# Performance work log

Hardware: AMD Instinct MI355X
Metric: run time of the kernel (lower is better)

Reference implementation:

```python
import jax, jax.numpy as jnp
import numpy as np

N = 100000
E = 1600000
IN_DIM = 128
OUT_DIM = 128
EDGE_DIM = 4
LN_EPS = 1e-5


def setup_inputs() -> dict:
    key = jax.random.key(0)
    ks = jax.random.split(key, 12)
    s_in = 1.0 / np.sqrt(IN_DIM)
    s_ed = 1.0 / np.sqrt(EDGE_DIM)
    s_out = 1.0 / np.sqrt(OUT_DIM)
    s_cat = 1.0 / np.sqrt(IN_DIM + OUT_DIM)
    return {
        "x": jax.random.normal(ks[0], (N, IN_DIM), jnp.float32),
        "edge_index": jax.random.randint(ks[1], (2, E), 0, N, jnp.int32),
        "edge_attr": jax.random.normal(ks[2], (E, EDGE_DIM), jnp.float32),
        # agg_mlp: Linear(in_dim, out_dim)
        "agg_W": jax.random.uniform(ks[3], (IN_DIM, OUT_DIM), jnp.float32, -s_in, s_in),
        "agg_b": jnp.zeros((OUT_DIM,), jnp.float32),
        # edge_mlp: Linear(edge_dim, out_dim) -> SiLU -> Linear(out_dim, 1) -> Sigmoid
        "edge_W1": jax.random.uniform(ks[4], (EDGE_DIM, OUT_DIM), jnp.float32, -s_ed, s_ed),
        "edge_b1": jnp.zeros((OUT_DIM,), jnp.float32),
        "edge_W2": jax.random.uniform(ks[5], (OUT_DIM, 1), jnp.float32, -s_out, s_out),
        "edge_b2": jnp.zeros((1,), jnp.float32),
        # update_mlp: Linear(in+out, out) -> SiLU -> Linear(out, out)
        "upd_W1": jax.random.uniform(ks[6], (IN_DIM + OUT_DIM, OUT_DIM), jnp.float32, -s_cat, s_cat),
        "upd_b1": jnp.zeros((OUT_DIM,), jnp.float32),
        "upd_W2": jax.random.uniform(ks[7], (OUT_DIM, OUT_DIM), jnp.float32, -s_out, s_out),
        "upd_b2": jnp.zeros((OUT_DIM,), jnp.float32),
        # LayerNorm(out_dim)
        "ln_g": jnp.ones((OUT_DIM,), jnp.float32),
        "ln_b": jnp.zeros((OUT_DIM,), jnp.float32),
        # residual: Linear(in_dim, out_dim, bias=False)
        "res_W": jax.random.uniform(ks[8], (IN_DIM, OUT_DIM), jnp.float32, -s_in, s_in),
    }


def reference(x, edge_index, edge_attr, agg_W, agg_b, edge_W1, edge_b1,
              edge_W2, edge_b2, upd_W1, upd_b1, upd_W2, upd_b2,
              ln_g, ln_b, res_W):
    n = x.shape[0]
    src, dst = edge_index[0], edge_index[1]
    # edge gate: (E, 1)
    e_h = jax.nn.silu(edge_attr @ edge_W1 + edge_b1)
    e_w = jax.nn.sigmoid(e_h @ edge_W2 + edge_b2)
    # gather -> gated message: (E, out_dim)
    x_agg = jax.nn.silu(x[src] @ agg_W + agg_b) * e_w
    # scatter-add mean aggregation
    out = jax.ops.segment_sum(x_agg, dst, num_segments=n)
    cnt = jax.ops.segment_sum(jnp.ones((dst.shape[0],), x.dtype), dst, num_segments=n)
    out = out / jnp.maximum(cnt, 1.0)[:, None]
    # update MLP on concat(x, aggregated)
    h = jnp.concatenate([x, out], axis=-1)
    h = jax.nn.silu(h @ upd_W1 + upd_b1) @ upd_W2 + upd_b2
    # residual + layernorm (dropout is identity in eval mode)
    h = h + x @ res_W
    mu = jnp.mean(h, axis=-1, keepdims=True)
    var = jnp.mean(jnp.square(h - mu), axis=-1, keepdims=True)
    h = (h - mu) * jax.lax.rsqrt(var + LN_EPS) * ln_g + ln_b
    return h
```

## Files before the change

kernel.cpp:

```cpp
#include <hip/hip_runtime.h>
#include <math.h>

#define N_NODES 100000
#define N_EDGES 1600000
#define LN_EPS 1e-5f

#define B_SHIFT 4
#define B_NODES 16
#define N_BUCKETS 6250
#define SEG_CAP 448

typedef __attribute__((ext_vector_type(8))) short short8;
typedef __attribute__((ext_vector_type(4))) float f32x4;
#define MFMA16(a, b, c) __builtin_amdgcn_mfma_f32_16x16x32_bf16(a, b, c, 0, 0, 0)

#define LOG2E 1.442695040888963f

#if __has_builtin(__builtin_amdgcn_exp2f) && __has_builtin(__builtin_amdgcn_rcpf)
__device__ __forceinline__ float sigmoidf_(float v) {
    return __builtin_amdgcn_rcpf(1.0f + __builtin_amdgcn_exp2f(-LOG2E * v));
}
#else
__device__ __forceinline__ float sigmoidf_(float v) { return 1.0f / (1.0f + __expf(-v)); }
#endif
__device__ __forceinline__ float siluf_(float v) { return v * sigmoidf_(v); }

__device__ __forceinline__ unsigned short f2bf_(float f) {
    unsigned int u = __float_as_uint(f);
    unsigned int rounded = u + 0x7FFF + ((u >> 16) & 1);
    return (unsigned short)(rounded >> 16);
}

__global__ __launch_bounds__(256) void kw(const float* __restrict__ W1,
                                          const float* __restrict__ W2,
                                          const float* __restrict__ resW,
                                          const float* __restrict__ aggW,
                                          unsigned short* __restrict__ w1t,
                                          unsigned short* __restrict__ w2t,
                                          unsigned short* __restrict__ rest,
                                          unsigned short* __restrict__ aggt,
                                          int* __restrict__ bcursor) {
    const int idx = blockIdx.x * 256 + threadIdx.x;
    if (idx < 32768) {
        const int n = idx >> 8, k = idx & 255;
        w1t[idx] = f2bf_(W1[k * 128 + n]);
    } else if (idx < 49152) {
        const int i = idx - 32768, n = i >> 7, k = i & 127;
        w2t[i] = f2bf_(W2[k * 128 + n]);
    } else if (idx < 65536) {
        const int i = idx - 49152, n = i >> 7, k = i & 127;
        rest[i] = f2bf_(resW[k * 128 + n]);
    } else if (idx < 81920) {
        const int i = idx - 65536, n = i >> 7, k = i & 127;
        aggt[i] = f2bf_(aggW[k * 128 + n]);
    } else if (idx < 81920 + N_BUCKETS) {
        const int n = idx - 81920;
        bcursor[n] = n * SEG_CAP;
    }
}

__global__ __launch_bounds__(256) void k1_y(const float* __restrict__ x,
                                            const unsigned short* __restrict__ aggt,
                                            const float* __restrict__ b,
                                            unsigned short* __restrict__ y16) {
    __shared__ unsigned short A1[32 * 136];
    __shared__ unsigned short O[32 * 136];
    const int t = threadIdx.x;
    const int n0 = blockIdx.x * 32;
    const float4* x4 = (const float4*)x;

#pragma unroll
    for (int r = 0; r < 4; ++r) {
        const int idx = t + r * 256;
        const int node = idx >> 5, c4 = idx & 31;
        const float4 v = x4[(n0 + node) * 32 + c4];
        ushort4 p;
        p.x = f2bf_(v.x); p.y = f2bf_(v.y); p.z = f2bf_(v.z); p.w = f2bf_(v.w);
        *(ushort4*)&A1[node * 136 + c4 * 4] = p;
    }
    __syncthreads();

    const int w = t >> 6, lane = t & 63, nq = lane & 15, quad = lane >> 4;
    f32x4 c[2][2] = {};
#pragma unroll
    for (int ks = 0; ks < 4; ++ks) {
        const int k0 = ks * 32 + quad * 8;
        const short8 a0 = *(const short8*)&A1[(nq)*136 + k0];
        const short8 a1 = *(const short8*)&A1[(16 + nq) * 136 + k0];
        const short8 b0 = *(const short8*)&aggt[(w * 32 + nq) * 128 + k0];
        const short8 b1 = *(const short8*)&aggt[(w * 32 + 16 + nq) * 128 + k0];
        c[0][0] = MFMA16(a0, b0, c[0][0]);
        c[0][1] = MFMA16(a0, b1, c[0][1]);
        c[1][0] = MFMA16(a1, b0, c[1][0]);
        c[1][1] = MFMA16(a1, b1, c[1][1]);
    }
    const float bc0 = b[w * 32 + nq], bc1 = b[w * 32 + 16 + nq];
#pragma unroll
    for (int mt = 0; mt < 2; ++mt)
#pragma unroll
        for (int r = 0; r < 4; ++r) {
            const int row = mt * 16 + quad * 4 + r;
            O[row * 136 + w * 32 + nq] = f2bf_(siluf_(c[mt][0][r] + bc0));
            O[row * 136 + w * 32 + 16 + nq] = f2bf_(siluf_(c[mt][1][r] + bc1));
        }
    __syncthreads();

#pragma unroll
    for (int r = 0; r < 2; ++r) {
        const int idx = t + r * 256;
        const int row = idx >> 4, c8 = idx & 15;
        const short8 v = *(const short8*)&O[row * 136 + c8 * 8];
        *(short8*)&y16[(n0 + row) * 128 + c8 * 8] = v;
    }
}

__global__ __launch_bounds__(128) void p3g(const float* __restrict__ attr,
                                           const float* __restrict__ W1,
                                           const float* __restrict__ b1,
                                           const float* __restrict__ W2,
                                           const float* __restrict__ b2,
                                           const int* __restrict__ src,
                                           const int* __restrict__ dst,
                                           int* __restrict__ bcursor,
                                           uint2* __restrict__ brec) {
    __shared__ float4 W1s[128];
    __shared__ float4 W2s[32];
    __shared__ float4 b1s[32];
    const int t = threadIdx.x;
    W1s[t] = ((const float4*)W1)[t];
    if (t < 32) {
        W2s[t] = ((const float4*)W2)[t];
        b1s[t] = ((const float4*)b1)[t];
    }
    __syncthreads();

    const int e0 = blockIdx.x * 256 + t;
    const int e1 = e0 + 128;
    const float4 a0 = ((const float4*)attr)[e0];
    const float4 a1 = ((const float4*)attr)[e1];
    const int s0 = src[e0], s1 = src[e1];
    const int d0 = dst[e0], d1 = dst[e1];
    float acc0 = 0.f, acc1 = 0.f;
#pragma unroll 8
    for (int j4 = 0; j4 < 32; ++j4) {
        const float4 r0 = W1s[j4];
        const float4 r1 = W1s[32 + j4];
        const float4 r2 = W1s[64 + j4];
        const float4 r3 = W1s[96 + j4];
        const float4 bb = b1s[j4];
        const float4 w2v = W2s[j4];
        float hx = fmaf(a0.x, r0.x, fmaf(a0.y, r1.x, fmaf(a0.z, r2.x, fmaf(a0.w, r3.x, bb.x))));
        float hy = fmaf(a0.x, r0.y, fmaf(a0.y, r1.y, fmaf(a0.z, r2.y, fmaf(a0.w, r3.y, bb.y))));
        float hz = fmaf(a0.x, r0.z, fmaf(a0.y, r1.z, fmaf(a0.z, r2.z, fmaf(a0.w, r3.z, bb.z))));
        float hw = fmaf(a0.x, r0.w, fmaf(a0.y, r1.w, fmaf(a0.z, r2.w, fmaf(a0.w, r3.w, bb.w))));
        float gx = fmaf(a1.x, r0.x, fmaf(a1.y, r1.x, fmaf(a1.z, r2.x, fmaf(a1.w, r3.x, bb.x))));
        float gy = fmaf(a1.x, r0.y, fmaf(a1.y, r1.y, fmaf(a1.z, r2.y, fmaf(a1.w, r3.y, bb.y))));
        float gz = fmaf(a1.x, r0.z, fmaf(a1.y, r1.z, fmaf(a1.z, r2.z, fmaf(a1.w, r3.z, bb.z))));
        float gw = fmaf(a1.x, r0.w, fmaf(a1.y, r1.w, fmaf(a1.z, r2.w, fmaf(a1.w, r3.w, bb.w))));
        acc0 = fmaf(siluf_(hx), w2v.x, acc0);
        acc1 = fmaf(siluf_(gx), w2v.x, acc1);
        acc0 = fmaf(siluf_(hy), w2v.y, acc0);
        acc1 = fmaf(siluf_(gy), w2v.y, acc1);
        acc0 = fmaf(siluf_(hz), w2v.z, acc0);
        acc1 = fmaf(siluf_(gz), w2v.z, acc1);
        acc0 = fmaf(siluf_(hw), w2v.w, acc0);
        acc1 = fmaf(siluf_(gw), w2v.w, acc1);
    }
    const float b2c = b2[0];
    const float ew0 = sigmoidf_(acc0 + b2c);
    const float ew1 = sigmoidf_(acc1 + b2c);
    const int bk0 = d0 >> B_SHIFT;
    const int slot0 = atomicAdd(&bcursor[bk0], 1);
    if (slot0 < (bk0 + 1) * SEG_CAP)
        brec[slot0] = make_uint2((unsigned)s0 | ((unsigned)(d0 & (B_NODES - 1)) << 27),
                                 __float_as_uint(ew0));
    const int bk1 = d1 >> B_SHIFT;
    const int slot1 = atomicAdd(&bcursor[bk1], 1);
    if (slot1 < (bk1 + 1) * SEG_CAP)
        brec[slot1] = make_uint2((unsigned)s1 | ((unsigned)(d1 & (B_NODES - 1)) << 27),
                                 __float_as_uint(ew1));
}

__global__ __launch_bounds__(512) void pB(const unsigned short* __restrict__ y16,
                                          const int* __restrict__ bcursor,
                                          const uint2* __restrict__ brec,
                                          float* __restrict__ agg) {
    __shared__ uint2 raw[SEG_CAP];
    __shared__ uint2 srec[SEG_CAP];
    __shared__ int hist[B_NODES];
    __shared__ int nstart[B_NODES];
    __shared__ int ncur[B_NODES];

    const int t = threadIdx.x;
    const int b = blockIdx.x;
    const int base = b * SEG_CAP;
    int c = bcursor[b] - base;
    if (c > SEG_CAP) c = SEG_CAP;

    if (t < B_NODES) hist[t] = 0;
    __syncthreads();

    for (int i = t; i < c; i += 512) {
        const uint2 r = brec[base + i];
        raw[i] = r;
        atomicAdd(&hist[r.x >> 27], 1);
    }
    __syncthreads();

    if (t == 0) {
        int acc = 0;
#pragma unroll
        for (int d = 0; d < B_NODES; ++d) {
            nstart[d] = acc;
            ncur[d] = acc;
            acc += hist[d];
        }
    }
    __syncthreads();

    for (int i = t; i < c; i += 512) {
        const uint2 r = raw[i];
        const int slot = atomicAdd(&ncur[r.x >> 27], 1);
        srec[slot] = r;
    }
    __syncthreads();

    const int w = t >> 6, lane = t & 63;
    const unsigned int* y32 = (const unsigned int*)y16;
#pragma unroll
    for (int rep = 0; rep < 2; ++rep) {
        const int d = w + rep * 8;
        const int st = nstart[d];
        const int cd = hist[d];
        const int end = st + cd;
        float ax0 = 0.f, ay0 = 0.f, ax1 = 0.f, ay1 = 0.f;
        float ax2 = 0.f, ay2 = 0.f, ax3 = 0.f, ay3 = 0.f;
        int p = st;
        for (; p + 8 <= end; p += 8) {
            const uint2 r0 = srec[p];
            const uint2 r1 = srec[p + 1];
            const uint2 r2 = srec[p + 2];
            const uint2 r3 = srec[p + 3];
            const uint2 r4 = srec[p + 4];
            const uint2 r5 = srec[p + 5];
            const uint2 r6 = srec[p + 6];
            const uint2 r7 = srec[p + 7];
            const unsigned int u0 = y32[(r0.x & 0x7FFFFFFu) * 64 + lane];
            const unsigned int u1 = y32[(r1.x & 0x7FFFFFFu) * 64 + lane];
            const unsigned int u2 = y32[(r2.x & 0x7FFFFFFu) * 64 + lane];
            const unsigned int u3 = y32[(r3.x & 0x7FFFFFFu) * 64 + lane];
            const unsigned int u4 = y32[(r4.x & 0x7FFFFFFu) * 64 + lane];
            const unsigned int u5 = y32[(r5.x & 0x7FFFFFFu) * 64 + lane];
            const unsigned int u6 = y32[(r6.x & 0x7FFFFFFu) * 64 + lane];
            const unsigned int u7 = y32[(r7.x & 0x7FFFFFFu) * 64 + lane];
            const float w0 = __uint_as_float(r0.y);
            const float w1 = __uint_as_float(r1.y);
            const float w2 = __uint_as_float(r2.y);
            const float w3 = __uint_as_float(r3.y);
            const float w4 = __uint_as_float(r4.y);
            const float w5 = __uint_as_float(r5.y);
            const float w6 = __uint_as_float(r6.y);
            const float w7 = __uint_as_float(r7.y);
            ax0 = fmaf(__uint_as_float(u0 << 16), w0, ax0);
            ay0 = fmaf(__uint_as_float(u0 & 0xFFFF0000u), w0, ay0);
            ax1 = fmaf(__uint_as_float(u1 << 16), w1, ax1);
            ay1 = fmaf(__uint_as_float(u1 & 0xFFFF0000u), w1, ay1);
            ax2 = fmaf(__uint_as_float(u2 << 16), w2, ax2);
            ay2 = fmaf(__uint_as_float(u2 & 0xFFFF0000u), w2, ay2);
            ax3 = fmaf(__uint_as_float(u3 << 16), w3, ax3);
            ay3 = fmaf(__uint_as_float(u3 & 0xFFFF0000u), w3, ay3);
            ax0 = fmaf(__uint_as_float(u4 << 16), w4, ax0);
            ay0 = fmaf(__uint_as_float(u4 & 0xFFFF0000u), w4, ay0);
            ax1 = fmaf(__uint_as_float(u5 << 16), w5, ax1);
            ay1 = fmaf(__uint_as_float(u5 & 0xFFFF0000u), w5, ay1);
            ax2 = fmaf(__uint_as_float(u6 << 16), w6, ax2);
            ay2 = fmaf(__uint_as_float(u6 & 0xFFFF0000u), w6, ay2);
            ax3 = fmaf(__uint_as_float(u7 << 16), w7, ax3);
            ay3 = fmaf(__uint_as_float(u7 & 0xFFFF0000u), w7, ay3);
        }
        for (; p + 4 <= end; p += 4) {
            const uint2 r0 = srec[p];
            const uint2 r1 = srec[p + 1];
            const uint2 r2 = srec[p + 2];
            const uint2 r3 = srec[p + 3];
            const unsigned int u0 = y32[(r0.x & 0x7FFFFFFu) * 64 + lane];
            const unsigned int u1 = y32[(r1.x & 0x7FFFFFFu) * 64 + lane];
            const unsigned int u2 = y32[(r2.x & 0x7FFFFFFu) * 64 + lane];
            const unsigned int u3 = y32[(r3.x & 0x7FFFFFFu) * 64 + lane];
            const float w0 = __uint_as_float(r0.y);
            const float w1 = __uint_as_float(r1.y);
            const float w2 = __uint_as_float(r2.y);
            const float w3 = __uint_as_float(r3.y);
            ax0 = fmaf(__uint_as_float(u0 << 16), w0, ax0);
            ay0 = fmaf(__uint_as_float(u0 & 0xFFFF0000u), w0, ay0);
            ax1 = fmaf(__uint_as_float(u1 << 16), w1, ax1);
            ay1 = fmaf(__uint_as_float(u1 & 0xFFFF0000u), w1, ay1);
            ax2 = fmaf(__uint_as_float(u2 << 16), w2, ax2);
            ay2 = fmaf(__uint_as_float(u2 & 0xFFFF0000u), w2, ay2);
            ax3 = fmaf(__uint_as_float(u3 << 16), w3, ax3);
            ay3 = fmaf(__uint_as_float(u3 & 0xFFFF0000u), w3, ay3);
        }
        for (; p < end; ++p) {
            const uint2 r0 = srec[p];
            const unsigned int u0 = y32[(r0.x & 0x7FFFFFFu) * 64 + lane];
            const float w0 = __uint_as_float(r0.y);
            ax0 = fmaf(__uint_as_float(u0 << 16), w0, ax0);
            ay0 = fmaf(__uint_as_float(u0 & 0xFFFF0000u), w0, ay0);
        }
        const float accx = (ax0 + ax1) + (ax2 + ax3);
        const float accy = (ay0 + ay1) + (ay2 + ay3);
        const float inv = 1.0f / fmaxf((float)cd, 1.0f);
        const int n = b * B_NODES + d;
        ((float2*)agg)[n * 64 + lane] = make_float2(accx * inv, accy * inv);
    }
}

__global__ __launch_bounds__(256) void k4_update(const float* __restrict__ x,
                                                 const float* agg,
                                                 const unsigned short* __restrict__ w1t,
                                                 const float* __restrict__ b1,
                                                 const unsigned short* __restrict__ w2t,
                                                 const float* __restrict__ b2,
                                                 const float* __restrict__ lng,
                                                 const float* __restrict__ lnb,
                                                 const unsigned short* __restrict__ rest,
                                                 float* out) {
    __shared__ unsigned short A1[32 * 264];
    __shared__ unsigned short A2[32 * 136];
    __shared__ float red_s[4][32];
    __shared__ float red_q[4][32];
    __shared__ float ln_mu[32];
    __shared__ float ln_rs[32];

    const int t = threadIdx.x;
    const int n0 = blockIdx.x * 32;
    const float4* x4 = (const float4*)x;
    const float4* agg4 = (const float4*)agg;

#pragma unroll
    for (int r = 0; r < 4; ++r) {
        const int idx = t + r * 256;
        const int node = idx >> 5, c4 = idx & 31;
        const float4 vx = x4[(n0 + node) * 32 + c4];
        const float4 va = agg4[(n0 + node) * 32 + c4];
        ushort4 px, pa;
        px.x = f2bf_(vx.x); px.y = f2bf_(vx.y); px.z = f2bf_(vx.z); px.w = f2bf_(vx.w);
        pa.x = f2bf_(va.x); pa.y = f2bf_(va.y); pa.z = f2bf_(va.z); pa.w = f2bf_(va.w);
        *(ushort4*)&A1[node * 264 + c4 * 4] = px;
        *(ushort4*)&A1[node * 264 + 128 + c4 * 4] = pa;
    }
    __syncthreads();

    const int w = t >> 6, lane = t & 63, nq = lane & 15, quad = lane >> 4;

    f32x4 c1[2][2] = {};
#pragma unroll
    for (int ks = 0; ks < 8; ++ks) {
        const int k0 = ks * 32 + quad * 8;
        const short8 a0 = *(const short8*)&A1[(nq)*264 + k0];
        const short8 a1 = *(const short8*)&A1[(16 + nq) * 264 + k0];
        const short8 b0 = *(const short8*)&w1t[(w * 32 + nq) * 256 + k0];
        const short8 b1f = *(const short8*)&w1t[(w * 32 + 16 + nq) * 256 + k0];
        c1[0][0] = MFMA16(a0, b0, c1[0][0]);
        c1[0][1] = MFMA16(a0, b1f, c1[0][1]);
        c1[1][0] = MFMA16(a1, b0, c1[1][0]);
        c1[1][1] = MFMA16(a1, b1f, c1[1][1]);
    }
    const float b1c0 = b1[w * 32 + nq], b1c1 = b1[w * 32 + 16 + nq];
#pragma unroll
    for (int mt = 0; mt < 2; ++mt)
#pragma unroll
        for (int r = 0; r < 4; ++r) {
            const int row = mt * 16 + quad * 4 + r;
            A2[row * 136 + w * 32 + nq] = f2bf_(siluf_(c1[mt][0][r] + b1c0));
            A2[row * 136 + w * 32 + 16 + nq] = f2bf_(siluf_(c1[mt][1][r] + b1c1));
        }
    __syncthreads();

    f32x4 c2[2][2] = {};
#pragma unroll
    for (int ks = 0; ks < 4; ++ks) {
        const int k0 = ks * 32 + quad * 8;
        const short8 a0 = *(const short8*)&A2[(nq)*136 + k0];
        const short8 a1 = *(const short8*)&A2[(16 + nq) * 136 + k0];
        const short8 b0 = *(const short8*)&w2t[(w * 32 + nq) * 128 + k0];
        const short8 b1f = *(const short8*)&w2t[(w * 32 + 16 + nq) * 128 + k0];
        c2[0][0] = MFMA16(a0, b0, c2[0][0]);
        c2[0][1] = MFMA16(a0, b1f, c2[0][1]);
        c2[1][0] = MFMA16(a1, b0, c2[1][0]);
        c2[1][1] = MFMA16(a1, b1f, c2[1][1]);
    }
#pragma unroll
    for (int ks = 0; ks < 4; ++ks) {
        const int k0 = ks * 32 + quad * 8;
        const short8 a0 = *(const short8*)&A1[(nq)*264 + k0];
        const short8 a1 = *(const short8*)&A1[(16 + nq) * 264 + k0];
        const short8 b0 = *(const short8*)&rest[(w * 32 + nq) * 128 + k0];
        const short8 b1f = *(const short8*)&rest[(w * 32 + 16 + nq) * 128 + k0];
        c2[0][0] = MFMA16(a0, b0, c2[0][0]);
        c2[0][1] = MFMA16(a0, b1f, c2[0][1]);
        c2[1][0] = MFMA16(a1, b0, c2[1][0]);
        c2[1][1] = MFMA16(a1, b1f, c2[1][1]);
    }

    const float b2c0 = b2[w * 32 + nq], b2c1 = b2[w * 32 + 16 + nq];
    float vals[2][2][4];
#pragma unroll
    for (int mt = 0; mt < 2; ++mt)
#pragma unroll
        for (int r = 0; r < 4; ++r) {
            vals[mt][0][r] = c2[mt][0][r] + b2c0;
            vals[mt][1][r] = c2[mt][1][r] + b2c1;
        }
#pragma unroll
    for (int mt = 0; mt < 2; ++mt)
#pragma unroll
        for (int r = 0; r < 4; ++r) {
            float s = vals[mt][0][r] + vals[mt][1][r];
            float q = vals[mt][0][r] * vals[mt][0][r] + vals[mt][1][r] * vals[mt][1][r];
#pragma unroll
            for (int off = 1; off <= 8; off <<= 1) {
                s += __shfl_xor(s, off, 64);
                q += __shfl_xor(q, off, 64);
            }
            if (nq == 0) {
                const int row = mt * 16 + quad * 4 + r;
                red_s[w][row] = s;
                red_q[w][row] = q;
            }
        }
    __syncthreads();
    if (t < 32) {
        const float ts = red_s[0][t] + red_s[1][t] + red_s[2][t] + red_s[3][t];
        const float tq = red_q[0][t] + red_q[1][t] + red_q[2][t] + red_q[3][t];
        const float mu = ts * (1.0f / 128.0f);
        const float var = fmaxf(tq * (1.0f / 128.0f) - mu * mu, 0.f);
        ln_mu[t] = mu;
        ln_rs[t] = rsqrtf(var + LN_EPS);
    }
    __syncthreads();

    const float g0 = lng[w * 32 + nq], g1 = lng[w * 32 + 16 + nq];
    const float lb0 = lnb[w * 32 + nq], lb1 = lnb[w * 32 + 16 + nq];
#pragma unroll
    for (int mt = 0; mt < 2; ++mt)
#pragma unroll
        for (int r = 0; r < 4; ++r) {
            const int row = mt * 16 + quad * 4 + r;
            const float mu = ln_mu[row], rs = ln_rs[row];
            out[(n0 + row) * 128 + w * 32 + nq] = (vals[mt][0][r] - mu) * rs * g0 + lb0;
            out[(n0 + row) * 128 + w * 32 + 16 + nq] = (vals[mt][1][r] - mu) * rs * g1 + lb1;
        }
}

extern "C" void kernel_launch(void* const* d_in, const int* in_sizes, int n_in,
                              void* d_out, int out_size, void* d_ws, size_t ws_size,
                              hipStream_t stream) {
    const float* x = (const float*)d_in[0];
    const int* ei = (const int*)d_in[1];
    const float* eattr = (const float*)d_in[2];
    const float* aggW = (const float*)d_in[3];
    const float* aggb = (const float*)d_in[4];
    const float* eW1 = (const float*)d_in[5];
    const float* eb1 = (const float*)d_in[6];
    const float* eW2 = (const float*)d_in[7];
    const float* eb2 = (const float*)d_in[8];
    const float* uW1 = (const float*)d_in[9];
    const float* ub1 = (const float*)d_in[10];
    const float* uW2 = (const float*)d_in[11];
    const float* ub2 = (const float*)d_in[12];
    const float* lng = (const float*)d_in[13];
    const float* lnb = (const float*)d_in[14];
    const float* resW = (const float*)d_in[15];
    float* out = (float*)d_out;

    char* ws = (char*)d_ws;
    unsigned short* y16 = (unsigned short*)(ws + 0);
    uint2* brec = (uint2*)(ws + 25600000);
    int* bcursor = (int*)(ws + 48000000);
    unsigned short* w1t = (unsigned short*)(ws + 48025008);
    unsigned short* w2t = (unsigned short*)(ws + 48090544);
    unsigned short* rest = (unsigned short*)(ws + 48123312);
    unsigned short* aggt = (unsigned short*)(ws + 48156080);
    float* agg = out;

    const int* src = ei;
    const int* dst = ei + N_EDGES;

    kw<<<346, 256, 0, stream>>>(uW1, uW2, resW, aggW, w1t, w2t, rest, aggt, bcursor);
    k1_y<<<N_NODES / 32, 256, 0, stream>>>(x, aggt, aggb, y16);
    p3g<<<N_EDGES / 256, 128, 0, stream>>>(eattr, eW1, eb1, eW2, eb2,
                                           src, dst, bcursor, brec);
    pB<<<N_BUCKETS, 512, 0, stream>>>(y16, bcursor, brec, agg);
    k4_update<<<N_NODES / 32, 256, 0, stream>>>(x, agg, w1t, ub1, w2t, ub2, lng, lnb, rest, out);
}
```

Measured before the change: 358.5 us.

## Split bucket sort and gather into separate kernels with column-sliced gather blocks

The fused per-bucket sort+gather kernel is split into pS, which sorts bucket records by destination and writes them back to global memory with per-node offsets, and pG, which runs eight blocks per bucket, each handling a 16-column slice. In pG each wavefront handles four nodes, with eight lane groups processing different edges in parallel, followed by a shuffle reduction. This is meant to raise parallelism and memory-level concurrency in the gather phase. In exchange it adds an extra kernel launch, a write and re-read of the sorted records, and eight reads of each bucket's record list. Each gather also becomes a 32-byte row segment instead of a full 256-byte coalesced row.

```diff
diff --git a/kernel.cpp b/kernel.cpp
--- a/kernel.cpp
+++ b/kernel.cpp
@@ -181,10 +181,9 @@
                                  __float_as_uint(ew1));
 }
 
-__global__ __launch_bounds__(512) void pB(const unsigned short* __restrict__ y16,
-                                          const int* __restrict__ bcursor,
-                                          const uint2* __restrict__ brec,
-                                          float* __restrict__ agg) {
+__global__ __launch_bounds__(256) void pS(const int* __restrict__ bcursor,
+                                          uint2* __restrict__ brec,
+                                          int* __restrict__ nmeta) {
     __shared__ uint2 raw[SEG_CAP];
     __shared__ uint2 srec[SEG_CAP];
     __shared__ int hist[B_NODES];
@@ -200,7 +199,7 @@
     if (t < B_NODES) hist[t] = 0;
     __syncthreads();
 
-    for (int i = t; i < c; i += 512) {
+    for (int i = t; i < c; i += 256) {
         const uint2 r = brec[base + i];
         raw[i] = r;
         atomicAdd(&hist[r.x >> 27], 1);
@@ -218,100 +217,62 @@
     }
     __syncthreads();
 
-    for (int i = t; i < c; i += 512) {
+    for (int i = t; i < c; i += 256) {
         const uint2 r = raw[i];
         const int slot = atomicAdd(&ncur[r.x >> 27], 1);
         srec[slot] = r;
     }
     __syncthreads();
 
+    for (int i = t; i < c; i += 256) brec[base + i] = srec[i];
+    if (t < B_NODES) nmeta[b * B_NODES + t] = nstart[t];
+}
+
+__global__ __launch_bounds__(256) void pG(const unsigned short* __restrict__ y16,
+                                          const int* __restrict__ bcursor,
+                                          const uint2* __restrict__ brec,
+                                          const int* __restrict__ nmeta,
+                                          float* __restrict__ agg) {
+    __shared__ int ns[B_NODES + 1];
+    const int t = threadIdx.x;
+    const int bid = blockIdx.x;
+    const int b = bid >> 3, g = bid & 7;
+    const int base = b * SEG_CAP;
+    if (t < B_NODES) ns[t] = nmeta[b * B_NODES + t];
+    if (t == B_NODES) {
+        int c = bcursor[b] - base;
+        ns[B_NODES] = (c > SEG_CAP) ? SEG_CAP : c;
+    }
+    __syncthreads();
+
     const int w = t >> 6, lane = t & 63;
+    const int rg = lane >> 3;
+    const int ui = lane & 7;
     const unsigned int* y32 = (const unsigned int*)y16;
-#pragma unroll
-    for (int rep = 0; rep < 2; ++rep) {
-        const int d = w + rep * 8;
-        const int st = nstart[d];
-        const int cd = hist[d];
-        const int end = st + cd;
-        float ax0 = 0.f, ay0 = 0.f, ax1 = 0.f, ay1 = 0.f;
-        float ax2 = 0.f, ay2 = 0.f, ax3 = 0.f, ay3 = 0.f;
-        int p = st;
-        for (; p + 8 <= end; p += 8) {
-            const uint2 r0 = srec[p];
-            const uint2 r1 = srec[p + 1];
-            const uint2 r2 = srec[p + 2];
-            const uint2 r3 = srec[p + 3];
-            const uint2 r4 = srec[p + 4];
-            const uint2 r5 = srec[p + 5];
-            const uint2 r6 = srec[p + 6];
-            const uint2 r7 = srec[p + 7];
-            const unsigned int u0 = y32[(r0.x & 0x7FFFFFFu) * 64 + lane];
-            const unsigned int u1 = y32[(r1.x & 0x7FFFFFFu) * 64 + lane];
-            const unsigned int u2 = y32[(r2.x & 0x7FFFFFFu) * 64 + lane];
-            const unsigned int u3 = y32[(r3.x & 0x7FFFFFFu) * 64 + lane];
-            const unsigned int u4 = y32[(r4.x & 0x7FFFFFFu) * 64 + lane];
-            const unsigned int u5 = y32[(r5.x & 0x7FFFFFFu) * 64 + lane];
-            const unsigned int u6 = y32[(r6.x & 0x7FFFFFFu) * 64 + lane];
-            const unsigned int u7 = y32[(r7.x & 0x7FFFFFFu) * 64 + lane];
-            const float w0 = __uint_as_float(r0.y);
-            const float w1 = __uint_as_float(r1.y);
-            const float w2 = __uint_as_float(r2.y);
-            const float w3 = __uint_as_float(r3.y);
-            const float w4 = __uint_as_float(r4.y);
-            const float w5 = __uint_as_float(r5.y);
-            const float w6 = __uint_as_float(r6.y);
-            const float w7 = __uint_as_float(r7.y);
-            ax0 = fmaf(__uint_as_float(u0 << 16), w0, ax0);
-            ay0 = fmaf(__uint_as_float(u0 & 0xFFFF0000u), w0, ay0);
-            ax1 = fmaf(__uint_as_float(u1 << 16), w1, ax1);
-            ay1 = fmaf(__uint_as_float(u1 & 0xFFFF0000u), w1, ay1);
-            ax2 = fmaf(__uint_as_float(u2 << 16), w2, ax2);
-            ay2 = fmaf(__uint_as_float(u2 & 0xFFFF0000u), w2, ay2);
-            ax3 = fmaf(__uint_as_float(u3 << 16), w3, ax3);
-            ay3 = fmaf(__uint_as_float(u3 & 0xFFFF0000u), w3, ay3);
-            ax0 = fmaf(__uint_as_float(u4 << 16), w4, ax0);
-            ay0 = fmaf(__uint_as_float(u4 & 0xFFFF0000u), w4, ay0);
-            ax1 = fmaf(__uint_as_float(u5 << 16), w5, ax1);
-            ay1 = fmaf(__uint_as_float(u5 & 0xFFFF0000u), w5, ay1);
-            ax2 = fmaf(__uint_as_float(u6 << 16), w6, ax2);
-            ay2 = fmaf(__uint_as_float(u6 & 0xFFFF0000u), w6, ay2);
-            ax3 = fmaf(__uint_as_float(u7 << 16), w7, ax3);
-            ay3 = fmaf(__uint_as_float(u7 & 0xFFFF0000u), w7, ay3);
-        }
-        for (; p + 4 <= end; p += 4) {
-            const uint2 r0 = srec[p];
-            const uint2 r1 = srec[p + 1];
-            const uint2 r2 = srec[p + 2];
-            const uint2 r3 = srec[p + 3];
-            const unsigned int u0 = y32[(r0.x & 0x7FFFFFFu) * 64 + lane];
-            const unsigned int u1 = y32[(r1.x & 0x7FFFFFFu) * 64 + lane];
-            const unsigned int u2 = y32[(r2.x & 0x7FFFFFFu) * 64 + lane];
-            const unsigned int u3 = y32[(r3.x & 0x7FFFFFFu) * 64 + lane];
-            const float w0 = __uint_as_float(r0.y);
-            const float w1 = __uint_as_float(r1.y);
-            const float w2 = __uint_as_float(r2.y);
-            const float w3 = __uint_as_float(r3.y);
-            ax0 = fmaf(__uint_as_float(u0 << 16), w0, ax0);
-            ay0 = fmaf(__uint_as_float(u0 & 0xFFFF0000u), w0, ay0);
-            ax1 = fmaf(__uint_as_float(u1 << 16), w1, ax1);
-            ay1 = fmaf(__uint_as_float(u1 & 0xFFFF0000u), w1, ay1);
-            ax2 = fmaf(__uint_as_float(u2 << 16), w2, ax2);
-            ay2 = fmaf(__uint_as_float(u2 & 0xFFFF0000u), w2, ay2);
-            ax3 = fmaf(__uint_as_float(u3 << 16), w3, ax3);
-            ay3 = fmaf(__uint_as_float(u3 & 0xFFFF0000u), w3, ay3);
-        }
-        for (; p < end; ++p) {
-            const uint2 r0 = srec[p];
-            const unsigned int u0 = y32[(r0.x & 0x7FFFFFFu) * 64 + lane];
-            const float w0 = __uint_as_float(r0.y);
-            ax0 = fmaf(__uint_as_float(u0 << 16), w0, ax0);
-            ay0 = fmaf(__uint_as_float(u0 & 0xFFFF0000u), w0, ay0);
-        }
-        const float accx = (ax0 + ax1) + (ax2 + ax3);
-        const float accy = (ay0 + ay1) + (ay2 + ay3);
-        const float inv = 1.0f / fmaxf((float)cd, 1.0f);
-        const int n = b * B_NODES + d;
-        ((float2*)agg)[n * 64 + lane] = make_float2(accx * inv, accy * inv);
+
+#pragma unroll
+    for (int rep = 0; rep < 4; ++rep) {
+        const int d = w * 4 + rep;
+        const int st = ns[d], end = ns[d + 1];
+        const int cd = end - st;
+        float ax = 0.f, ay = 0.f;
+        for (int p = st + rg; p < end; p += 8) {
+            const uint2 r = brec[base + p];
+            const unsigned int u = y32[(r.x & 0x7FFFFFFu) * 64 + g * 8 + ui];
+            const float wgt = __uint_as_float(r.y);
+            ax = fmaf(__uint_as_float(u << 16), wgt, ax);
+            ay = fmaf(__uint_as_float(u & 0xFFFF0000u), wgt, ay);
+        }
+#pragma unroll
+        for (int off = 8; off < 64; off <<= 1) {
+            ax += __shfl_xor(ax, off, 64);
+            ay += __shfl_xor(ay, off, 64);
+        }
+        if (lane < 8) {
+            const float inv = 1.0f / fmaxf((float)cd, 1.0f);
+            ((float2*)agg)[(b * B_NODES + d) * 64 + g * 8 + lane] =
+                make_float2(ax * inv, ay * inv);
+        }
     }
 }
 
@@ -482,6 +443,7 @@
     unsigned short* w2t = (unsigned short*)(ws + 48090544);
     unsigned short* rest = (unsigned short*)(ws + 48123312);
     unsigned short* aggt = (unsigned short*)(ws + 48156080);
+    int* nmeta = (int*)(ws + 48188848);
     float* agg = out;
 
     const int* src = ei;
@@ -491,6 +453,7 @@
     k1_y<<<N_NODES / 32, 256, 0, stream>>>(x, aggt, aggb, y16);
     p3g<<<N_EDGES / 256, 128, 0, stream>>>(eattr, eW1, eb1, eW2, eb2,
                                            src, dst, bcursor, brec);
-    pB<<<N_BUCKETS, 512, 0, stream>>>(y16, bcursor, brec, agg);
+    pS<<<N_BUCKETS, 256, 0, stream>>>(bcursor, brec, nmeta);
+    pG<<<N_BUCKETS * 8, 256, 0, stream>>>(y16, bcursor, brec, nmeta, agg);
     k4_update<<<N_NODES / 32, 256, 0, stream>>>(x, agg, w1t, ub1, w2t, ub2, lng, lnb, rest, out);
 }
```

Measured after the change: 534.6 us. 1.49x slower.
